# Optimization experiments

Measured on AMD Instinct MI355X. Metric: run time of the kernel, lower is better.

The kernel has to match this reference:

```python
import jax, jax.numpy as jnp
import numpy as np

DIM, HIDDEN, E = 1024, 4096, 8
B, L = 2, 2048


def setup_inputs() -> dict:
    key = jax.random.key(0)
    ks = jax.random.split(key, 6)
    s_in = 1.0 / np.sqrt(DIM)
    s_h = 1.0 / np.sqrt(HIDDEN)
    return {
        "x": jax.random.normal(ks[0], (B, L, DIM), dtype=jnp.float32),
        "Wg": jax.random.uniform(ks[1], (E, DIM), jnp.float32, -s_in, s_in),
        "W1": jax.random.uniform(ks[2], (E, DIM, HIDDEN), jnp.float32, -s_in, s_in),
        "b1": jax.random.uniform(ks[3], (E, HIDDEN), jnp.float32, -s_in, s_in),
        "W2": jax.random.uniform(ks[4], (E, HIDDEN, DIM), jnp.float32, -s_h, s_h),
        "b2": jax.random.uniform(ks[5], (E, DIM), jnp.float32, -s_h, s_h),
    }


def reference(x, Wg, W1, b1, W2, b2):
    # Router: top-1 over gate logits (softmax is monotone, argmax of probs == argmax of logits)
    gate_logits = jnp.einsum("bld,ed->ble", x, Wg)  # [B, L, E]
    top1 = jnp.argmax(gate_logits, axis=-1)          # [B, L] int
    out = jnp.zeros_like(x)
    # Fixed small loop over experts (structurally distinct weights); per-expert
    # dense MLP + select, honoring top-1 dispatch/combine semantics.
    for e in range(E):
        mask = (top1 == e)[..., None]                                   # [B, L, 1]
        h = jax.nn.gelu(jnp.einsum("bld,dh->blh", x, W1[e]) + b1[e],
                        approximate=False)                              # [B, L, H]
        y = jnp.einsum("blh,hd->bld", h, W2[e]) + b2[e]                 # [B, L, D]
        out = jnp.where(mask, y, out)
    return out
```

## Files before the change

### kernel.cpp

```cpp
#include <hip/hip_runtime.h>
#include <hip/hip_bf16.h>
#include <math.h>

#define NTOK 4096
#define DIMSZ 1024
#define HID 4096
#define NE 8
#define RT_MAX 40

typedef unsigned short u16;
typedef unsigned int u32;
typedef __attribute__((ext_vector_type(8))) short bf16x8;
typedef __attribute__((ext_vector_type(4))) float f32x4;

static __device__ __forceinline__ u16 f2bf(float f) {
    u32 u = __float_as_uint(f);
    u32 r = u + 0x7fffu + ((u >> 16) & 1u);
    return (u16)(r >> 16);
}

static __device__ __forceinline__ u32 pk2bf(float lo, float hi) {
    __hip_bfloat162 h = __float22bfloat162_rn(make_float2(lo, hi));
    return *(u32*)&h;
}

__global__ void k_init(int* counts, int* cursor) {
    if (threadIdx.x < NE) { counts[threadIdx.x] = 0; cursor[threadIdx.x] = 0; }
}

__global__ __launch_bounds__(256) void k_router(const float* __restrict__ x,
                                                const float* __restrict__ Wg,
                                                int* __restrict__ ids,
                                                int* __restrict__ counts) {
    int wave = threadIdx.x >> 6;
    int lane = threadIdx.x & 63;
    int t = blockIdx.x * 4 + wave;

    const float4* xr = (const float4*)(x + (size_t)t * DIMSZ);
    float4 xv[4];
#pragma unroll
    for (int j = 0; j < 4; j++) xv[j] = xr[j * 64 + lane];

    float s[NE];
#pragma unroll
    for (int e = 0; e < NE; e++) {
        const float4* wr = (const float4*)(Wg + (size_t)e * DIMSZ);
        float p = 0.f;
#pragma unroll
        for (int j = 0; j < 4; j++) {
            float4 w = wr[j * 64 + lane];
            p += xv[j].x * w.x + xv[j].y * w.y + xv[j].z * w.z + xv[j].w * w.w;
        }
#pragma unroll
        for (int m = 32; m >= 1; m >>= 1) p += __shfl_xor(p, m, 64);
        s[e] = p;
    }
    if (lane == 0) {
        int best = 0;
#pragma unroll
        for (int e = 1; e < NE; e++) if (s[e] > s[best]) best = e;
        ids[t] = best;
        atomicAdd(&counts[best], 1);
    }
}

__global__ void k_scan(const int* __restrict__ counts, int* __restrict__ offs) {
    if (threadIdx.x == 0) {
        int a = 0;
        for (int e = 0; e < NE; e++) { offs[e] = a; a += counts[e]; }
    }
}

__global__ __launch_bounds__(256) void k_gather(const float* __restrict__ x,
                                                const int* __restrict__ ids,
                                                const int* __restrict__ offs,
                                                int* __restrict__ cursor,
                                                int* __restrict__ perm,
                                                u16* __restrict__ Xg) {
    int t = blockIdx.x;
    __shared__ int sp;
    if (threadIdx.x == 0) {
        int e = ids[t];
        int p = offs[e] + atomicAdd(&cursor[e], 1);
        perm[p] = t;
        sp = p;
    }
    __syncthreads();
    int p = sp;
    const float4* src = (const float4*)(x + (size_t)t * DIMSZ);
    float4 v = src[threadIdx.x];
    u32 w0 = pk2bf(v.x, v.y);
    u32 w1 = pk2bf(v.z, v.w);
    uint2* dst = (uint2*)(Xg + (size_t)p * DIMSZ + threadIdx.x * 4);
    *dst = make_uint2(w0, w1);
}

template <int KDIM, int NDIM, int EPI>
__global__ __launch_bounds__(256) void k_gemm(const u16* __restrict__ A,
                                              const float* __restrict__ Ball,
                                              const float* __restrict__ biasAll,
                                              const int* __restrict__ counts,
                                              const int* __restrict__ offs,
                                              const int* __restrict__ perm,
                                              u16* __restrict__ Hout,
                                              float* __restrict__ Fout) {
    constexpr int NT = NDIM / 128;
    constexpr int NWG = RT_MAX * NT;
    constexpr int CPX = NWG / 8;
    constexpr int NK = KDIM / 64;
    int bid = blockIdx.x;
    int wid = (bid & 7) * CPX + (bid >> 3);
    int x = wid % RT_MAX;
    int n0 = (wid / RT_MAX) * 128;

    int e = -1, lrt = 0, a0 = 0;
#pragma unroll
    for (int i = 0; i < NE; i++) {
        int rt = (counts[i] + 127) >> 7;
        if (e < 0 && x < a0 + rt) { e = i; lrt = x - a0; }
        a0 += rt;
    }
    if (e < 0) return;
    int row0 = offs[e] + lrt * 128;
    int nrows = offs[e] + counts[e] - row0;
    if (nrows > 128) nrows = 128;

    __shared__ alignas(16) u16 Asb[3][128][64];
    __shared__ alignas(16) u16 Bsb[2][128][64];

    int tid = threadIdx.x;
    int lane = tid & 63;
    int wave = tid >> 6;
    int wr = wave >> 1, wc = wave & 1;

    const u16* srcA[4];
#pragma unroll
    for (int p = 0; p < 4; p++) {
        int g = p * 256 + tid;
        int r = g >> 3, slot = g & 7;
        int rc = r < nrows ? r : nrows - 1;
        srcA[p] = A + (size_t)(row0 + rc) * KDIM + ((slot ^ (r & 7)) * 8);
    }
    int bn4 = (tid & 31) * 4;
    int bkb = tid >> 5;
    const float* srcB = Ball + (size_t)e * KDIM * NDIM + (size_t)(bkb * 8) * NDIM + n0 + bn4;

    f32x4 acc[4][4] = {};
    int fr = lane & 15, fc = lane >> 4;

    float4 breg[8];
    u16 *Ar = &Asb[0][0][0], *An = &Asb[1][0][0], *Aw = &Asb[2][0][0];
    u16 *Br = &Bsb[0][0][0], *Bw = &Bsb[1][0][0];

#define LOAD_B(KT)                                                              \
    {                                                                           \
        const float* bp = srcB + (size_t)(KT) * 64 * NDIM;                      \
        _Pragma("unroll")                                                       \
        for (int j = 0; j < 8; j++) breg[j] = *(const float4*)(bp + (size_t)j * NDIM); \
    }

#define STAGE_A(DST, KT)                                                        \
    {                                                                           \
        _Pragma("unroll")                                                       \
        for (int p = 0; p < 4; p++) {                                           \
            __builtin_amdgcn_global_load_lds(                                   \
                (const __attribute__((address_space(1))) void*)(srcA[p] + (KT) * 64), \
                (__attribute__((address_space(3))) void*)((DST) + (p * 256 + wave * 64) * 8), \
                16, 0, 0);                                                      \
        }                                                                       \
    }

#define WRITE_B(DST)                                                            \
    {                                                                           \
        const float* vf = (const float*)breg;                                   \
        _Pragma("unroll")                                                       \
        for (int i = 0; i < 4; i++) {                                           \
            int N = bn4 + i;                                                    \
            u32 w0 = pk2bf(vf[0 + i],  vf[4 + i]);                              \
            u32 w1 = pk2bf(vf[8 + i],  vf[12 + i]);                             \
            u32 w2 = pk2bf(vf[16 + i], vf[20 + i]);                             \
            u32 w3 = pk2bf(vf[24 + i], vf[28 + i]);                             \
            u32 off = (u32)(bkb * 16) ^ (u32)((N & 7) << 4);                    \
            *(uint4*)((char*)(DST) + N * 128 + off) = make_uint4(w0, w1, w2, w3); \
        }                                                                       \
    }

#define COMPUTE()                                                               \
    {                                                                           \
        _Pragma("unroll")                                                       \
        for (int k2 = 0; k2 < 2; k2++) {                                        \
            bf16x8 af[4], bfr[4];                                               \
            _Pragma("unroll")                                                   \
            for (int m = 0; m < 4; m++) {                                       \
                int r = wr * 64 + m * 16 + fr;                                  \
                u32 off = (u32)(k2 * 64 + fc * 16) ^ (u32)((r & 7) << 4);       \
                af[m] = *(const bf16x8*)((const char*)Ar + r * 128 + off);      \
            }                                                                   \
            _Pragma("unroll")                                                   \
            for (int n = 0; n < 4; n++) {                                       \
                int N = wc * 64 + n * 16 + fr;                                  \
                u32 off = (u32)(k2 * 64 + fc * 16) ^ (u32)((N & 7) << 4);       \
                bfr[n] = *(const bf16x8*)((const char*)Br + N * 128 + off);     \
            }                                                                   \
            _Pragma("unroll")                                                   \
            for (int m = 0; m < 4; m++)                                         \
                _Pragma("unroll")                                               \
                for (int n = 0; n < 4; n++)                                     \
                    acc[m][n] = __builtin_amdgcn_mfma_f32_16x16x32_bf16(af[m], bfr[n], acc[m][n], 0, 0, 0); \
        }                                                                       \
    }

#define WAITV(N) asm volatile("s_waitcnt vmcnt(" #N ")" ::: "memory")
#define WAITL()  asm volatile("s_waitcnt lgkmcnt(0)" ::: "memory")
#define BAR()    __builtin_amdgcn_s_barrier()

    LOAD_B(0);
    STAGE_A(Ar, 0);
    WAITV(4);
    WRITE_B(Br);
    LOAD_B(1);
    STAGE_A(An, 1);
    WAITV(12);
    WAITL();
    BAR();

    for (int kk = 0; kk < NK - 2; kk++) {
        COMPUTE();
        WAITV(4);
        WRITE_B(Bw);
        LOAD_B(kk + 2);
        STAGE_A(Aw, kk + 2);
        WAITV(12);
        WAITL();
        BAR();
        u16* t = Ar; Ar = An; An = Aw; Aw = t;
        t = Br; Br = Bw; Bw = t;
    }
    COMPUTE();
    WAITV(4);
    WRITE_B(Bw);
    WAITV(0);
    WAITL();
    BAR();
    { u16* t = Ar; Ar = An; An = Aw; Aw = t; t = Br; Br = Bw; Bw = t; }
    COMPUTE();

#undef LOAD_B
#undef STAGE_A
#undef WRITE_B
#undef COMPUTE
#undef WAITV
#undef WAITL
#undef BAR

    int cb = lane & 15;
    int rq = lane >> 4;
#pragma unroll
    for (int m = 0; m < 4; m++) {
        int rbase = wr * 64 + m * 16 + rq * 4;
#pragma unroll
        for (int n = 0; n < 4; n++) {
            int col = n0 + wc * 64 + n * 16 + cb;
            float bias = biasAll[(size_t)e * NDIM + col];
#pragma unroll
            for (int j = 0; j < 4; j++) {
                int r = rbase + j;
                if (r < nrows) {
                    float v = acc[m][n][j] + bias;
                    int p = row0 + r;
                    if (EPI == 1) {
                        float g = 0.5f * v * (1.0f + erff(v * 0.70710678118654752f));
                        Hout[(size_t)p * NDIM + col] = f2bf(g);
                    } else {
                        int trow = perm[p];
                        Fout[(size_t)trow * NDIM + col] = v;
                    }
                }
            }
        }
    }
}

extern "C" void kernel_launch(void* const* d_in, const int* in_sizes, int n_in,
                              void* d_out, int out_size, void* d_ws, size_t ws_size,
                              hipStream_t stream) {
    const float* x  = (const float*)d_in[0];
    const float* Wg = (const float*)d_in[1];
    const float* W1 = (const float*)d_in[2];
    const float* b1 = (const float*)d_in[3];
    const float* W2 = (const float*)d_in[4];
    const float* b2 = (const float*)d_in[5];
    float* out = (float*)d_out;

    char* ws = (char*)d_ws;
    int* ids    = (int*)(ws + 0);
    int* counts = (int*)(ws + 16384);
    int* offs   = (int*)(ws + 16448);
    int* cursor = (int*)(ws + 16512);
    int* perm   = (int*)(ws + 16576);
    u16* Xg     = (u16*)(ws + 33024);
    u16* H      = (u16*)(ws + 33024 + 8388608);

    k_init<<<dim3(1), dim3(64), 0, stream>>>(counts, cursor);
    k_router<<<dim3(NTOK / 4), dim3(256), 0, stream>>>(x, Wg, ids, counts);
    k_scan<<<dim3(1), dim3(64), 0, stream>>>(counts, offs);
    k_gather<<<dim3(NTOK), dim3(256), 0, stream>>>(x, ids, offs, cursor, perm, Xg);
    k_gemm<DIMSZ, HID, 1><<<dim3(RT_MAX * (HID / 128)), dim3(256), 0, stream>>>(
        Xg, W1, b1, counts, offs, perm, H, (float*)nullptr);
    k_gemm<HID, DIMSZ, 2><<<dim3(RT_MAX * (DIMSZ / 128)), dim3(256), 0, stream>>>(
        H, W2, b2, counts, offs, perm, (u16*)nullptr, out);
}
```

Before: 311.4 us.

## Pre-transpose weights to bf16, split-K second GEMM with atomics

Adds a kernel that converts W1 and W2 to transposed bf16 copies in workspace on every call. Both GEMMs can then stage B tiles straight into LDS with global_load_lds instead of loading fp32 and converting in registers. The second GEMM is split four ways along K and accumulates into a pre-zeroed output with atomicAdd. The new GEMM uses a simple single-buffered 32-wide K loop with two barriers per step and occupancy hint 4. This costs an extra full pass over the weights, float atomics and a zeroing kernel, and falls back to the old path (now with a different swizzle) when the workspace is too small.

```diff
diff --git a/kernel.cpp b/kernel.cpp
--- a/kernel.cpp
+++ b/kernel.cpp
@@ -26,6 +26,11 @@
 
 __global__ void k_init(int* counts, int* cursor) {
     if (threadIdx.x < NE) { counts[threadIdx.x] = 0; cursor[threadIdx.x] = 0; }
+}
+
+__global__ void k_zero(float* p) {
+    int i = blockIdx.x * 1024 + threadIdx.x * 4;
+    *(float4*)(p + i) = make_float4(0.f, 0.f, 0.f, 0.f);
 }
 
 __global__ __launch_bounds__(256) void k_router(const float* __restrict__ x,
@@ -95,15 +100,181 @@
     *dst = make_uint2(w0, w1);
 }
 
+__global__ __launch_bounds__(256) void k_wt(const float* __restrict__ W1,
+                                            const float* __restrict__ W2,
+                                            u16* __restrict__ W1T,
+                                            u16* __restrict__ W2T) {
+    int bid = blockIdx.x;
+    const float* src;
+    u16* dst;
+    int K, N, kt, nt;
+    if (bid < 8192) {
+        int e = bid >> 10, t = bid & 1023;
+        kt = t >> 6; nt = t & 63;
+        src = W1 + (size_t)e * 1024 * 4096;
+        dst = W1T + (size_t)e * 4096 * 1024;
+        K = 1024; N = 4096;
+    } else {
+        int b = bid - 8192;
+        int e = b >> 10, t = b & 1023;
+        kt = t >> 4; nt = t & 15;
+        src = W2 + (size_t)e * 4096 * 1024;
+        dst = W2T + (size_t)e * 1024 * 4096;
+        K = 4096; N = 1024;
+    }
+    __shared__ u32 T[32][65];
+    int tid = threadIdx.x;
+#pragma unroll
+    for (int pass = 0; pass < 2; pass++) {
+        int kp = (tid >> 4) + pass * 16;
+        int nc = (tid & 15) * 4;
+        const float* r0 = src + (size_t)(kt * 64 + 2 * kp) * N + nt * 64 + nc;
+        float4 a = *(const float4*)r0;
+        float4 b = *(const float4*)(r0 + N);
+        T[kp][nc + 0] = pk2bf(a.x, b.x);
+        T[kp][nc + 1] = pk2bf(a.y, b.y);
+        T[kp][nc + 2] = pk2bf(a.z, b.z);
+        T[kp][nc + 3] = pk2bf(a.w, b.w);
+    }
+    __syncthreads();
+    int n = tid >> 2;
+    int sb = (tid & 3) * 8;
+    u16* orow = dst + (size_t)(nt * 64 + n) * K + kt * 64;
+#pragma unroll
+    for (int p = 0; p < 2; p++) {
+        int s = sb + p * 4;
+        uint4 w = make_uint4(T[s][n], T[s + 1][n], T[s + 2][n], T[s + 3][n]);
+        *(uint4*)(orow + 2 * s) = w;
+    }
+}
+
+template <int KDIM, int NDIM, int EPI, int KSPLIT>
+__global__ __launch_bounds__(256, 4) void k_gemm(const u16* __restrict__ A,
+                                                 const u16* __restrict__ Wt,
+                                                 const float* __restrict__ biasAll,
+                                                 const int* __restrict__ counts,
+                                                 const int* __restrict__ offs,
+                                                 const int* __restrict__ perm,
+                                                 u16* __restrict__ Hout,
+                                                 float* __restrict__ Fout) {
+    constexpr int NT = NDIM / 128;
+    constexpr int NWG = RT_MAX * NT * KSPLIT;
+    constexpr int CPX = NWG / 8;
+    constexpr int KL = KDIM / KSPLIT;
+    constexpr int NKL = KL / 32;
+    int bid = blockIdx.x;
+    int wid = (bid & 7) * CPX + (bid >> 3);
+    int x = wid % RT_MAX;
+    int rest = wid / RT_MAX;
+    int ks = rest % KSPLIT;
+    int n0 = (rest / KSPLIT) * 128;
+    int kbase = ks * KL;
+
+    int e = -1, lrt = 0, a0 = 0;
+#pragma unroll
+    for (int i = 0; i < NE; i++) {
+        int rt = (counts[i] + 127) >> 7;
+        if (e < 0 && x < a0 + rt) { e = i; lrt = x - a0; }
+        a0 += rt;
+    }
+    if (e < 0) return;
+    int row0 = offs[e] + lrt * 128;
+    int nrows = offs[e] + counts[e] - row0;
+    if (nrows > 128) nrows = 128;
+
+    __shared__ alignas(16) u16 As[128][32];
+    __shared__ alignas(16) u16 Bs[128][32];
+
+    int tid = threadIdx.x;
+    int lane = tid & 63;
+    int wave = tid >> 6;
+    int wr = wave >> 1, wc = wave & 1;
+
+    const u16* srcA[2];
+    const u16* srcB[2];
+#pragma unroll
+    for (int p = 0; p < 2; p++) {
+        int g = p * 256 + tid;
+        int r = g >> 2, slot = g & 3;
+        int rc = r < nrows ? r : nrows - 1;
+        int kg = (slot ^ (r & 3)) * 8;
+        srcA[p] = A + (size_t)(row0 + rc) * KDIM + kbase + kg;
+        srcB[p] = Wt + (size_t)e * NDIM * KDIM + (size_t)(n0 + r) * KDIM + kbase + kg;
+    }
+
+    f32x4 acc[4][4] = {};
+    int fr = lane & 15, fc = lane >> 4;
+
+    for (int kk = 0; kk < NKL; kk++) {
+#pragma unroll
+        for (int p = 0; p < 2; p++) {
+            __builtin_amdgcn_global_load_lds(
+                (const __attribute__((address_space(1))) void*)(srcA[p] + kk * 32),
+                (__attribute__((address_space(3))) void*)((u16*)&As[0][0] + (p * 256 + wave * 64) * 8),
+                16, 0, 0);
+            __builtin_amdgcn_global_load_lds(
+                (const __attribute__((address_space(1))) void*)(srcB[p] + kk * 32),
+                (__attribute__((address_space(3))) void*)((u16*)&Bs[0][0] + (p * 256 + wave * 64) * 8),
+                16, 0, 0);
+        }
+        __syncthreads();
+        bf16x8 af[4], bfr[4];
+#pragma unroll
+        for (int m = 0; m < 4; m++) {
+            int r = wr * 64 + m * 16 + fr;
+            af[m] = *(const bf16x8*)&As[r][(fc ^ (r & 3)) * 8];
+        }
+#pragma unroll
+        for (int n = 0; n < 4; n++) {
+            int N = wc * 64 + n * 16 + fr;
+            bfr[n] = *(const bf16x8*)&Bs[N][(fc ^ (N & 3)) * 8];
+        }
+#pragma unroll
+        for (int m = 0; m < 4; m++)
+#pragma unroll
+            for (int n = 0; n < 4; n++)
+                acc[m][n] = __builtin_amdgcn_mfma_f32_16x16x32_bf16(af[m], bfr[n], acc[m][n], 0, 0, 0);
+        __syncthreads();
+    }
+
+    int cb = lane & 15;
+    int rq = lane >> 4;
+#pragma unroll
+    for (int m = 0; m < 4; m++) {
+        int rbase = wr * 64 + m * 16 + rq * 4;
+#pragma unroll
+        for (int n = 0; n < 4; n++) {
+            int col = n0 + wc * 64 + n * 16 + cb;
+            float bias = (EPI == 2 && ks != 0) ? 0.f : biasAll[(size_t)e * NDIM + col];
+#pragma unroll
+            for (int j = 0; j < 4; j++) {
+                int r = rbase + j;
+                if (r < nrows) {
+                    float v = acc[m][n][j] + bias;
+                    int p = row0 + r;
+                    if (EPI == 1) {
+                        float g = 0.5f * v * (1.0f + erff(v * 0.70710678118654752f));
+                        Hout[(size_t)p * NDIM + col] = f2bf(g);
+                    } else {
+                        int trow = perm[p];
+                        atomicAdd(&Fout[(size_t)trow * NDIM + col], v);
+                    }
+                }
+            }
+        }
+    }
+}
+
 template <int KDIM, int NDIM, int EPI>
-__global__ __launch_bounds__(256) void k_gemm(const u16* __restrict__ A,
-                                              const float* __restrict__ Ball,
-                                              const float* __restrict__ biasAll,
-                                              const int* __restrict__ counts,
-                                              const int* __restrict__ offs,
-                                              const int* __restrict__ perm,
-                                              u16* __restrict__ Hout,
-                                              float* __restrict__ Fout) {
+__global__ __launch_bounds__(256) void k_gemm_rs(const u16* __restrict__ A,
+                                                 const float* __restrict__ Ball,
+                                                 const float* __restrict__ biasAll,
+                                                 const int* __restrict__ counts,
+                                                 const int* __restrict__ offs,
+                                                 const int* __restrict__ perm,
+                                                 u16* __restrict__ Hout,
+                                                 float* __restrict__ Fout) {
+#define S8(r) ((((r) ^ ((r) >> 3))) & 7)
     constexpr int NT = NDIM / 128;
     constexpr int NWG = RT_MAX * NT;
     constexpr int CPX = NWG / 8;
@@ -139,7 +310,7 @@
         int g = p * 256 + tid;
         int r = g >> 3, slot = g & 7;
         int rc = r < nrows ? r : nrows - 1;
-        srcA[p] = A + (size_t)(row0 + rc) * KDIM + ((slot ^ (r & 7)) * 8);
+        srcA[p] = A + (size_t)(row0 + rc) * KDIM + ((slot ^ S8(r)) * 8);
     }
     int bn4 = (tid & 31) * 4;
     int bkb = tid >> 5;
@@ -158,7 +329,6 @@
         _Pragma("unroll")                                                       \
         for (int j = 0; j < 8; j++) breg[j] = *(const float4*)(bp + (size_t)j * NDIM); \
     }
-
 #define STAGE_A(DST, KT)                                                        \
     {                                                                           \
         _Pragma("unroll")                                                       \
@@ -169,7 +339,6 @@
                 16, 0, 0);                                                      \
         }                                                                       \
     }
-
 #define WRITE_B(DST)                                                            \
     {                                                                           \
         const float* vf = (const float*)breg;                                   \
@@ -180,11 +349,10 @@
             u32 w1 = pk2bf(vf[8 + i],  vf[12 + i]);                             \
             u32 w2 = pk2bf(vf[16 + i], vf[20 + i]);                             \
             u32 w3 = pk2bf(vf[24 + i], vf[28 + i]);                             \
-            u32 off = (u32)(bkb * 16) ^ (u32)((N & 7) << 4);                    \
+            u32 off = (u32)(bkb * 16) ^ (u32)(S8(N) << 4);                      \
             *(uint4*)((char*)(DST) + N * 128 + off) = make_uint4(w0, w1, w2, w3); \
         }                                                                       \
     }
-
 #define COMPUTE()                                                               \
     {                                                                           \
         _Pragma("unroll")                                                       \
@@ -193,13 +361,13 @@
             _Pragma("unroll")                                                   \
             for (int m = 0; m < 4; m++) {                                       \
                 int r = wr * 64 + m * 16 + fr;                                  \
-                u32 off = (u32)(k2 * 64 + fc * 16) ^ (u32)((r & 7) << 4);       \
+                u32 off = (u32)(k2 * 64 + fc * 16) ^ (u32)(S8(r) << 4);         \
                 af[m] = *(const bf16x8*)((const char*)Ar + r * 128 + off);      \
             }                                                                   \
             _Pragma("unroll")                                                   \
             for (int n = 0; n < 4; n++) {                                       \
                 int N = wc * 64 + n * 16 + fr;                                  \
-                u32 off = (u32)(k2 * 64 + fc * 16) ^ (u32)((N & 7) << 4);       \
+                u32 off = (u32)(k2 * 64 + fc * 16) ^ (u32)(S8(N) << 4);         \
                 bfr[n] = *(const bf16x8*)((const char*)Br + N * 128 + off);     \
             }                                                                   \
             _Pragma("unroll")                                                   \
@@ -209,7 +377,6 @@
                     acc[m][n] = __builtin_amdgcn_mfma_f32_16x16x32_bf16(af[m], bfr[n], acc[m][n], 0, 0, 0); \
         }                                                                       \
     }
-
 #define WAITV(N) asm volatile("s_waitcnt vmcnt(" #N ")" ::: "memory")
 #define WAITL()  asm volatile("s_waitcnt lgkmcnt(0)" ::: "memory")
 #define BAR()    __builtin_amdgcn_s_barrier()
@@ -252,6 +419,7 @@
 #undef WAITV
 #undef WAITL
 #undef BAR
+#undef S8
 
     int cb = lane & 15;
     int rq = lane >> 4;
@@ -298,15 +466,32 @@
     int* offs   = (int*)(ws + 16448);
     int* cursor = (int*)(ws + 16512);
     int* perm   = (int*)(ws + 16576);
-    u16* Xg     = (u16*)(ws + 33024);
-    u16* H      = (u16*)(ws + 33024 + 8388608);
+
+    u16* XgN  = (u16*)(ws + 65536);
+    u16* HN   = (u16*)(ws + 65536 + 8388608);
+    u16* W1T  = (u16*)(ws + 65536 + 8388608 + 33554432);
+    u16* W2T  = (u16*)(ws + 65536 + 8388608 + 33554432 + 67108864);
+    const size_t NEED = 65536ull + 8388608 + 33554432 + 67108864 + 67108864;
 
     k_init<<<dim3(1), dim3(64), 0, stream>>>(counts, cursor);
     k_router<<<dim3(NTOK / 4), dim3(256), 0, stream>>>(x, Wg, ids, counts);
     k_scan<<<dim3(1), dim3(64), 0, stream>>>(counts, offs);
-    k_gather<<<dim3(NTOK), dim3(256), 0, stream>>>(x, ids, offs, cursor, perm, Xg);
-    k_gemm<DIMSZ, HID, 1><<<dim3(RT_MAX * (HID / 128)), dim3(256), 0, stream>>>(
-        Xg, W1, b1, counts, offs, perm, H, (float*)nullptr);
-    k_gemm<HID, DIMSZ, 2><<<dim3(RT_MAX * (DIMSZ / 128)), dim3(256), 0, stream>>>(
-        H, W2, b2, counts, offs, perm, (u16*)nullptr, out);
-}
+
+    if (ws_size >= NEED) {
+        k_gather<<<dim3(NTOK), dim3(256), 0, stream>>>(x, ids, offs, cursor, perm, XgN);
+        k_wt<<<dim3(16384), dim3(256), 0, stream>>>(W1, W2, W1T, W2T);
+        k_zero<<<dim3(NTOK * DIMSZ / 1024), dim3(256), 0, stream>>>(out);
+        k_gemm<DIMSZ, HID, 1, 1><<<dim3(RT_MAX * (HID / 128)), dim3(256), 0, stream>>>(
+            XgN, W1T, b1, counts, offs, perm, HN, (float*)nullptr);
+        k_gemm<HID, DIMSZ, 2, 4><<<dim3(RT_MAX * (DIMSZ / 128) * 4), dim3(256), 0, stream>>>(
+            HN, W2T, b2, counts, offs, perm, (u16*)nullptr, out);
+    } else {
+        u16* Xg = (u16*)(ws + 33024);
+        u16* H  = (u16*)(ws + 33024 + 8388608);
+        k_gather<<<dim3(NTOK), dim3(256), 0, stream>>>(x, ids, offs, cursor, perm, Xg);
+        k_gemm_rs<DIMSZ, HID, 1><<<dim3(RT_MAX * (HID / 128)), dim3(256), 0, stream>>>(
+            Xg, W1, b1, counts, offs, perm, H, (float*)nullptr);
+        k_gemm_rs<HID, DIMSZ, 2><<<dim3(RT_MAX * (DIMSZ / 128)), dim3(256), 0, stream>>>(
+            H, W2, b2, counts, offs, perm, (u16*)nullptr, out);
+    }
+}
```

Result: slower. 408.8 us (+31.3%).
